# Performance work log

Measured on AMD Instinct MI355X. Metric: run time of the kernel, lower is better.

## Reference

```python
import jax, jax.numpy as jnp
import numpy as np

VOCAB, EMB = 100000, 50
KERNEL_NUM, SIGMA, EXACT_SIGMA = 21, 0.1, 0.001
OUT_LAYERS = [10, 5]


def _kernel_params():
    # Mirrors KNRM._get_kernels_layers
    mus = [1.0]
    bin_size = 2.0 / (KERNEL_NUM - 1)
    mus.append(1 - bin_size / 2)
    for i in range(1, KERNEL_NUM - 1):
        mus.append(mus[i] - bin_size)
    mus = list(reversed(mus))
    sigmas = [SIGMA] * (KERNEL_NUM - 1) + [EXACT_SIGMA]
    return np.array(mus, np.float32), np.array(sigmas, np.float32)

MUS, SIGMAS = _kernel_params()


def setup_inputs() -> dict:
    key = jax.random.key(0)
    ks = jax.random.split(key, 12)
    B, LQ, LD = 2048, 32, 256
    emb = jax.random.normal(ks[0], (VOCAB, EMB), jnp.float32)
    emb = emb.at[0].set(0.0)  # padding_idx=0
    query1 = jax.random.randint(ks[1], (B, LQ), 0, VOCAB)
    doc1 = jax.random.randint(ks[2], (B, LD), 0, VOCAB)
    query2 = jax.random.randint(ks[3], (B, LQ), 0, VOCAB)
    doc2 = jax.random.randint(ks[4], (B, LD), 0, VOCAB)
    def lin(k, fan_in, fan_out):
        bound = 1.0 / np.sqrt(fan_in)
        kw, kb = jax.random.split(k)
        w = jax.random.uniform(kw, (fan_out, fan_in), jnp.float32, -bound, bound)
        b = jax.random.uniform(kb, (fan_out,), jnp.float32, -bound, bound)
        return w, b
    w0, b0 = lin(ks[5], KERNEL_NUM, OUT_LAYERS[0])
    w1, b1 = lin(ks[6], OUT_LAYERS[0], OUT_LAYERS[1])
    w2, b2 = lin(ks[7], OUT_LAYERS[1], 1)
    return dict(emb=emb, w0=w0, b0=b0, w1=w1, b1=b1, w2=w2, b2=b2,
                query1=query1, doc1=doc1, query2=query2, doc2=doc2)


def _matching_matrix(emb, query, doc):
    qe = emb[query]                     # [B, Lq, E]
    de = emb[doc]                       # [B, Ld, E]
    qn = qe / (jnp.linalg.norm(qe, axis=-1, keepdims=True) + 1e-13)
    dn = de / (jnp.linalg.norm(de, axis=-1, keepdims=True) + 1e-13)
    return jnp.einsum('bqe,bde->bqd', qn, dn)  # cosine sim [B, Lq, Ld]


def _apply_kernels(mm):
    # Loop over the fixed 21 kernels (structurally distinct mu/sigma),
    # avoiding a [B,Lq,Ld,21] intermediate, as the original does.
    km = []
    for mu, sg in zip(MUS, SIGMAS):
        k = jnp.exp(-(mm - mu) ** 2 / (2.0 * sg * sg))
        km.append(jnp.log1p(k.sum(axis=-1)).sum(axis=-1))  # [B]
    return jnp.stack(km, axis=1)  # [B, K]


def _mlp(x, w0, b0, w1, b1, w2, b2):
    h = jax.nn.relu(x @ w0.T + b0)
    h = jax.nn.relu(h @ w1.T + b1)
    return h @ w2.T + b2  # [B, 1]


def _predict(emb, w0, b0, w1, b1, w2, b2, query, doc):
    mm = _matching_matrix(emb, query, doc)
    ko = _apply_kernels(mm)
    return _mlp(ko, w0, b0, w1, b1, w2, b2)


def reference(emb, w0, b0, w1, b1, w2, b2, query1, doc1, query2, doc2):
    logits1 = _predict(emb, w0, b0, w1, b1, w2, b2, query1, doc1)
    logits2 = _predict(emb, w0, b0, w1, b1, w2, b2, query2, doc2)
    return jax.nn.sigmoid(logits1 - logits2)  # [B, 1]
```

## Files before the change

kernel.cpp:

```cpp
#include <hip/hip_runtime.h>
#include <hip/hip_fp16.h>

#define EMB_N 50
#define KP 64
#define LQ 32
#define LD 256
#define KN 21
#define MMH 36
#define BATCH 2048

typedef short v8s __attribute__((ext_vector_type(8)));
typedef float v4f __attribute__((ext_vector_type(4)));
typedef float v2f __attribute__((ext_vector_type(2)));

#define PK_ACC(d, b)    asm("v_pk_add_f32 %0, %0, %1" : "+v"(d) : "v"(b))
#define PK_MULA(d, b)   asm("v_pk_mul_f32 %0, %0, %1" : "+v"(d) : "v"(b))

__device__ inline short bf16_rne(float f) {
  unsigned u = __float_as_uint(f);
  unsigned r = u + 0x7fffu + ((u >> 16) & 1u);
  return (short)(r >> 16);
}
__device__ inline float bf16_tof(short h) {
  return __uint_as_float(((unsigned)(unsigned short)h) << 16);
}

__global__ __launch_bounds__(256) void vocab_norm_kernel(
    const float* __restrict__ emb, short* __restrict__ vb,
    short* __restrict__ vlo, int vocab)
{
  int gid = blockIdx.x * 256 + threadIdx.x;
  int r = gid >> 3;
  int c = gid & 7;
  if (r >= vocab) return;
  const float* row = emb + (size_t)r * EMB_N;
  float v[8];
#pragma unroll
  for (int k = 0; k < 8; k++) v[k] = 0.f;
  float ss = 0.f;
  int e0 = c * 8;
  if (c < 6) {
    const float2* p = (const float2*)(row + e0);
#pragma unroll
    for (int k = 0; k < 4; k++) {
      float2 t = p[k];
      v[2*k] = t.x; v[2*k+1] = t.y;
      ss = fmaf(t.x, t.x, ss); ss = fmaf(t.y, t.y, ss);
    }
  } else if (c == 6) {
    float2 t = *(const float2*)(row + 48);
    v[0] = t.x; v[1] = t.y;
    ss = fmaf(t.x, t.x, t.y * t.y);
  }
  ss += __shfl_xor(ss, 1);
  ss += __shfl_xor(ss, 2);
  ss += __shfl_xor(ss, 4);
  float inv = 1.0f / (sqrtf(ss) + 1e-13f);
  short hi[8], lo[8];
#pragma unroll
  for (int k = 0; k < 8; k++) {
    float f = v[k] * inv;
    hi[k] = bf16_rne(f);
    lo[k] = bf16_rne(f - bf16_tof(hi[k]));
  }
  size_t o = (size_t)r * KP + e0;
  *(uint4*)(vb + o)  = *(const uint4*)hi;
  *(uint4*)(vlo + o) = *(const uint4*)lo;
}

__device__ __constant__ const float CJ[KN] = {
  2.5261639e-20f, 2.0469719e-16f, 6.1019363e-13f, 6.6915861e-10f, 2.6995785e-7f,
  4.0065297e-5f,  2.1874911e-3f,  4.3936937e-2f,  0.32465247f,    0.88249690f,
  0.88249690f,    0.32465247f,    4.3936937e-2f,  2.1874911e-3f,  4.0065297e-5f,
  2.6995785e-7f,  6.6915861e-10f, 6.1019363e-13f, 2.0469719e-16f, 2.5261639e-20f,
  1.0f
};

__global__ __launch_bounds__(256, 6) void knrm_main_kernel(
    const short* __restrict__ vb, const short* __restrict__ vlo,
    const int* __restrict__ q1, const int* __restrict__ d1,
    const int* __restrict__ q2, const int* __restrict__ d2,
    const float* __restrict__ w0, const float* __restrict__ b0,
    const float* __restrict__ w1, const float* __restrict__ b1,
    const float* __restrict__ w2, const float* __restrict__ b2,
    float* __restrict__ lgbuf)
{
  __shared__ unsigned short mmh[LD * MMH];
  __shared__ float Sq[LQ][KN + 1];
  __shared__ float ko[KN];
  __shared__ float h0s[10];
  __shared__ float h1s[5];

  const int pair = blockIdx.x >> 11;
  const int b = blockIdx.x & (BATCH - 1);
  const int tid = threadIdx.x;
  const int wave = tid >> 6;
  const int lane = tid & 63;
  const int l15 = lane & 15;
  const int quad = lane >> 4;

  const int* qp = pair ? q2 : q1;
  const int* dp = pair ? d2 : d1;

  if (tid < KN) ko[tid] = 0.f;
  if (tid < LQ) Sq[tid][20] = 0.f;

  int mydtok = dp[b * LD + tid];

  const int mtile = wave & 1;
  const int n0 = (wave >> 1) * 8;

  int qtok = qp[b * LQ + mtile * 16 + l15];
  const short* qh = vb  + (size_t)qtok * KP + quad * 8;
  const short* ql = vlo + (size_t)qtok * KP + quad * 8;
  v8s Ah0 = *(const v8s*)(qh);
  v8s Ah1 = *(const v8s*)(qh + 32);
  v8s Al0 = *(const v8s*)(ql);
  v8s Al1 = *(const v8s*)(ql + 32);

  int dtoks[8];
#pragma unroll
  for (int n = 0; n < 8; n++)
    dtoks[n] = dp[b * LD + (n0 + n) * 16 + l15];

#pragma unroll 2
  for (int n = 0; n < 8; n++) {
    int dtok = dtoks[n];
    const short* dh = vb + (size_t)dtok * KP + quad * 8;
    v8s B0 = *(const v8s*)(dh);
    v8s B1 = *(const v8s*)(dh + 32);
    v4f C = {0.f, 0.f, 0.f, 0.f};
    C = __builtin_amdgcn_mfma_f32_16x16x32_bf16(Ah0, B0, C, 0, 0, 0);
    C = __builtin_amdgcn_mfma_f32_16x16x32_bf16(Ah1, B1, C, 0, 0, 0);
    C = __builtin_amdgcn_mfma_f32_16x16x32_bf16(Al0, B0, C, 0, 0, 0);
    C = __builtin_amdgcn_mfma_f32_16x16x32_bf16(Al1, B1, C, 0, 0, 0);
    int col = (n0 + n) * 16 + l15;
    int row0 = mtile * 16 + quad * 4;
    __half2 h01 = __floats2half2_rn(C[0], C[1]);
    __half2 h23 = __floats2half2_rn(C[2], C[3]);
    uint2 wpk;
    wpk.x = *reinterpret_cast<unsigned*>(&h01);
    wpk.y = *reinterpret_cast<unsigned*>(&h23);
    *(uint2*)&mmh[col * MMH + row0] = wpk;
  }
  __syncthreads();

#pragma unroll
  for (int qq = 0; qq < LQ; qq++) {
    int qt = qp[b * LQ + qq];
    unsigned long long m = __ballot(mydtok == qt && qt != 0);
    if (lane == 0 && m)
      atomicAdd(&Sq[qq][20], (float)__popcll(m));
  }

  const int q  = tid >> 3;
  const int db = tid & 7;
  v2f U2[10];
#pragma unroll
  for (int i = 0; i < 10; i++) U2[i] = (v2f){0.f, 0.f};

#pragma unroll 4
  for (int i = 0; i < LD / 8; i++) {
    float x = __half2float(*reinterpret_cast<const __half*>(
                  &mmh[(db + 8 * i) * MMH + q]));
    float gc = __builtin_amdgcn_exp2f(x * fmaf(-72.1347520f, x, 7.2134752f));
    float ex = 14.4269504f * x;
    float r  = __builtin_amdgcn_exp2f(ex);
    float ri = __builtin_amdgcn_exp2f(-ex);
    v2f p  = {gc, gc * ri};
    v2f rr = {r, ri};
#pragma unroll
    for (int k2 = 0; k2 < 10; k2++) {
      PK_ACC(U2[k2], p);
      PK_MULA(p, rr);
    }
  }

#pragma unroll
  for (int j = 0; j < 20; j++) {
    float v = (j < 10) ? U2[9 - j].y : U2[j - 10].x;
    v += __shfl_xor(v, 1);
    v += __shfl_xor(v, 2);
    v += __shfl_xor(v, 4);
    if (db == 0) Sq[q][j] = v;
  }
  __syncthreads();

  {
    int qq = tid & 31;
    int jb = tid >> 5;
#pragma unroll
    for (int k = 0; k < 3; k++) {
      int j = jb + 8 * k;
      if (j < KN) {
        float y = fmaf(CJ[j], Sq[qq][j], 1.0f);
        float l = 0.69314718f * __builtin_amdgcn_logf(y);
        atomicAdd(&ko[j], l);
      }
    }
  }
  __syncthreads();

  if (tid < 10) {
    float h = b0[tid];
#pragma unroll
    for (int k = 0; k < KN; k++) h = fmaf(w0[tid * KN + k], ko[k], h);
    h0s[tid] = fmaxf(h, 0.f);
  }
  __syncthreads();
  if (tid < 5) {
    float h = b1[tid];
#pragma unroll
    for (int k = 0; k < 10; k++) h = fmaf(w1[tid * 10 + k], h0s[k], h);
    h1s[tid] = fmaxf(h, 0.f);
  }
  __syncthreads();
  if (tid == 0) {
    float h = b2[0];
#pragma unroll
    for (int k = 0; k < 5; k++) h = fmaf(w2[k], h1s[k], h);
    lgbuf[pair * BATCH + b] = h;
  }
}

__global__ __launch_bounds__(256) void knrm_combine_kernel(
    const float* __restrict__ lgbuf, float* __restrict__ out)
{
  int i = blockIdx.x * 256 + threadIdx.x;
  if (i < BATCH) {
    float z = lgbuf[i] - lgbuf[BATCH + i];
    out[i] = 1.0f / (1.0f + expf(-z));
  }
}

extern "C" void kernel_launch(void* const* d_in, const int* in_sizes, int n_in,
                              void* d_out, int out_size, void* d_ws, size_t ws_size,
                              hipStream_t stream)
{
  const float* emb = (const float*)d_in[0];
  const float* w0  = (const float*)d_in[1];
  const float* b0  = (const float*)d_in[2];
  const float* w1  = (const float*)d_in[3];
  const float* b1  = (const float*)d_in[4];
  const float* w2  = (const float*)d_in[5];
  const float* b2  = (const float*)d_in[6];
  const int* q1 = (const int*)d_in[7];
  const int* dd1 = (const int*)d_in[8];
  const int* q2 = (const int*)d_in[9];
  const int* dd2 = (const int*)d_in[10];
  float* out = (float*)d_out;

  int vocab = in_sizes[0] / EMB_N;
  int B = in_sizes[7] / LQ;

  float* lgbuf = (float*)d_ws;
  short* vb  = (short*)(lgbuf + 2 * BATCH);
  short* vlo = vb + (size_t)vocab * KP;

  vocab_norm_kernel<<<(vocab * 8 + 255) / 256, 256, 0, stream>>>(emb, vb, vlo, vocab);
  knrm_main_kernel<<<2 * B, 256, 0, stream>>>(vb, vlo, q1, dd1, q2, dd2,
                                              w0, b0, w1, b1, w2, b2, lgbuf);
  knrm_combine_kernel<<<(B + 255) / 256, 256, 0, stream>>>(lgbuf, out);
}
```

Measured before the change: 157.7 us.

## Fuse kernel-pooling into MFMA loop, drop shared similarity matrix

The kernel no longer stores the fp16 cosine-similarity matrix in shared memory and re-reads it. Each wave now applies the Gaussian kernel accumulation directly to its MFMA output registers. Operand roles are swapped so doc tokens are the A operand, and the next doc embedding is prefetched while the current one is processed. Partial sums are reduced with cross-lane shuffles into a small shared array, and the log-sum into ko uses shuffle reductions instead of shared atomics. The occupancy hint drops from 6 to 5 because register pressure rises, and every element now goes through the exp work in fp32 rather than via a half-precision round trip.

```diff
diff --git a/kernel.cpp b/kernel.cpp
--- a/kernel.cpp
+++ b/kernel.cpp
@@ -1,12 +1,10 @@
 #include <hip/hip_runtime.h>
-#include <hip/hip_fp16.h>
 
 #define EMB_N 50
 #define KP 64
 #define LQ 32
 #define LD 256
 #define KN 21
-#define MMH 36
 #define BATCH 2048
 
 typedef short v8s __attribute__((ext_vector_type(8)));
@@ -76,7 +74,7 @@
   1.0f
 };
 
-__global__ __launch_bounds__(256, 6) void knrm_main_kernel(
+__global__ __launch_bounds__(256, 5) void knrm_main_kernel(
     const short* __restrict__ vb, const short* __restrict__ vlo,
     const int* __restrict__ q1, const int* __restrict__ d1,
     const int* __restrict__ q2, const int* __restrict__ d2,
@@ -85,8 +83,8 @@
     const float* __restrict__ w2, const float* __restrict__ b2,
     float* __restrict__ lgbuf)
 {
-  __shared__ unsigned short mmh[LD * MMH];
-  __shared__ float Sq[LQ][KN + 1];
+  __shared__ float part[4][16][KN];
+  __shared__ float Sqex[LQ];
   __shared__ float ko[KN];
   __shared__ float h0s[10];
   __shared__ float h1s[5];
@@ -98,51 +96,28 @@
   const int lane = tid & 63;
   const int l15 = lane & 15;
   const int quad = lane >> 4;
+  const int qtile = wave >> 1;
+  const int thalf = wave & 1;
 
   const int* qp = pair ? q2 : q1;
   const int* dp = pair ? d2 : d1;
 
-  if (tid < KN) ko[tid] = 0.f;
-  if (tid < LQ) Sq[tid][20] = 0.f;
-
-  int mydtok = dp[b * LD + tid];
-
-  const int mtile = wave & 1;
-  const int n0 = (wave >> 1) * 8;
-
-  int qtok = qp[b * LQ + mtile * 16 + l15];
+  if (tid < LQ) Sqex[tid] = 0.f;
+
+  int qtok = qp[b * LQ + qtile * 16 + l15];
   const short* qh = vb  + (size_t)qtok * KP + quad * 8;
   const short* ql = vlo + (size_t)qtok * KP + quad * 8;
-  v8s Ah0 = *(const v8s*)(qh);
-  v8s Ah1 = *(const v8s*)(qh + 32);
-  v8s Al0 = *(const v8s*)(ql);
-  v8s Al1 = *(const v8s*)(ql + 32);
-
+  v8s Bh0 = *(const v8s*)(qh);
+  v8s Bh1 = *(const v8s*)(qh + 32);
+  v8s Bl0 = *(const v8s*)(ql);
+  v8s Bl1 = *(const v8s*)(ql + 32);
+
+  int mydtok = dp[b * LD + tid];
   int dtoks[8];
 #pragma unroll
-  for (int n = 0; n < 8; n++)
-    dtoks[n] = dp[b * LD + (n0 + n) * 16 + l15];
-
-#pragma unroll 2
-  for (int n = 0; n < 8; n++) {
-    int dtok = dtoks[n];
-    const short* dh = vb + (size_t)dtok * KP + quad * 8;
-    v8s B0 = *(const v8s*)(dh);
-    v8s B1 = *(const v8s*)(dh + 32);
-    v4f C = {0.f, 0.f, 0.f, 0.f};
-    C = __builtin_amdgcn_mfma_f32_16x16x32_bf16(Ah0, B0, C, 0, 0, 0);
-    C = __builtin_amdgcn_mfma_f32_16x16x32_bf16(Ah1, B1, C, 0, 0, 0);
-    C = __builtin_amdgcn_mfma_f32_16x16x32_bf16(Al0, B0, C, 0, 0, 0);
-    C = __builtin_amdgcn_mfma_f32_16x16x32_bf16(Al1, B1, C, 0, 0, 0);
-    int col = (n0 + n) * 16 + l15;
-    int row0 = mtile * 16 + quad * 4;
-    __half2 h01 = __floats2half2_rn(C[0], C[1]);
-    __half2 h23 = __floats2half2_rn(C[2], C[3]);
-    uint2 wpk;
-    wpk.x = *reinterpret_cast<unsigned*>(&h01);
-    wpk.y = *reinterpret_cast<unsigned*>(&h23);
-    *(uint2*)&mmh[col * MMH + row0] = wpk;
-  }
+  for (int t = 0; t < 8; t++)
+    dtoks[t] = dp[b * LD + (thalf * 8 + t) * 16 + l15];
+
   __syncthreads();
 
 #pragma unroll
@@ -150,53 +125,78 @@
     int qt = qp[b * LQ + qq];
     unsigned long long m = __ballot(mydtok == qt && qt != 0);
     if (lane == 0 && m)
-      atomicAdd(&Sq[qq][20], (float)__popcll(m));
-  }
-
-  const int q  = tid >> 3;
-  const int db = tid & 7;
+      atomicAdd(&Sqex[qq], (float)__popcll(m));
+  }
+
   v2f U2[10];
 #pragma unroll
   for (int i = 0; i < 10; i++) U2[i] = (v2f){0.f, 0.f};
 
-#pragma unroll 4
-  for (int i = 0; i < LD / 8; i++) {
-    float x = __half2float(*reinterpret_cast<const __half*>(
-                  &mmh[(db + 8 * i) * MMH + q]));
-    float gc = __builtin_amdgcn_exp2f(x * fmaf(-72.1347520f, x, 7.2134752f));
-    float ex = 14.4269504f * x;
-    float r  = __builtin_amdgcn_exp2f(ex);
-    float ri = __builtin_amdgcn_exp2f(-ex);
-    v2f p  = {gc, gc * ri};
-    v2f rr = {r, ri};
-#pragma unroll
-    for (int k2 = 0; k2 < 10; k2++) {
-      PK_ACC(U2[k2], p);
-      PK_MULA(p, rr);
-    }
-  }
-
-#pragma unroll
-  for (int j = 0; j < 20; j++) {
-    float v = (j < 10) ? U2[9 - j].y : U2[j - 10].x;
-    v += __shfl_xor(v, 1);
-    v += __shfl_xor(v, 2);
-    v += __shfl_xor(v, 4);
-    if (db == 0) Sq[q][j] = v;
+  const short* dptr0 = vb + (size_t)dtoks[0] * KP + quad * 8;
+  v8s A0 = *(const v8s*)(dptr0);
+  v8s A1 = *(const v8s*)(dptr0 + 32);
+
+#pragma unroll 2
+  for (int t = 0; t < 8; t++) {
+    v8s N0, N1;
+    if (t < 7) {
+      const short* dptr = vb + (size_t)dtoks[t + 1] * KP + quad * 8;
+      N0 = *(const v8s*)(dptr);
+      N1 = *(const v8s*)(dptr + 32);
+    }
+    v4f C = {0.f, 0.f, 0.f, 0.f};
+    C = __builtin_amdgcn_mfma_f32_16x16x32_bf16(A0, Bh0, C, 0, 0, 0);
+    C = __builtin_amdgcn_mfma_f32_16x16x32_bf16(A1, Bh1, C, 0, 0, 0);
+    C = __builtin_amdgcn_mfma_f32_16x16x32_bf16(A0, Bl0, C, 0, 0, 0);
+    C = __builtin_amdgcn_mfma_f32_16x16x32_bf16(A1, Bl1, C, 0, 0, 0);
+#pragma unroll
+    for (int r = 0; r < 4; r++) {
+      float x = C[r];
+      float gc = __builtin_amdgcn_exp2f(x * fmaf(-72.1347520f, x, 7.2134752f));
+      float ex = 14.4269504f * x;
+      float rr1 = __builtin_amdgcn_exp2f(ex);
+      float ri  = __builtin_amdgcn_exp2f(-ex);
+      v2f p  = {gc, gc * ri};
+      v2f rr = {rr1, ri};
+#pragma unroll
+      for (int k2 = 0; k2 < 10; k2++) {
+        PK_ACC(U2[k2], p);
+        PK_MULA(p, rr);
+      }
+    }
+    if (t < 7) { A0 = N0; A1 = N1; }
+  }
+
+#pragma unroll
+  for (int i = 0; i < 10; i++) {
+    float ux = U2[i].x, uy = U2[i].y;
+    ux += __shfl_xor(ux, 16);  uy += __shfl_xor(uy, 16);
+    ux += __shfl_xor(ux, 32);  uy += __shfl_xor(uy, 32);
+    if (quad == 0) {
+      part[wave][l15][10 + i] = ux;
+      part[wave][l15][9 - i]  = uy;
+    }
   }
   __syncthreads();
 
   {
     int qq = tid & 31;
+    int qi = qq & 15, qt2 = qq >> 4;
     int jb = tid >> 5;
 #pragma unroll
     for (int k = 0; k < 3; k++) {
       int j = jb + 8 * k;
+      float l = 0.f;
       if (j < KN) {
-        float y = fmaf(CJ[j], Sq[qq][j], 1.0f);
-        float l = 0.69314718f * __builtin_amdgcn_logf(y);
-        atomicAdd(&ko[j], l);
+        float s = (j < 20) ? part[qt2 * 2][qi][j] + part[qt2 * 2 + 1][qi][j]
+                           : Sqex[qq];
+        float y = fmaf(CJ[j], s, 1.0f);
+        l = 0.69314718f * __builtin_amdgcn_logf(y);
       }
+      l += __shfl_xor(l, 1);  l += __shfl_xor(l, 2);
+      l += __shfl_xor(l, 4);  l += __shfl_xor(l, 8);
+      l += __shfl_xor(l, 16);
+      if (qq == 0 && j < KN) ko[j] = l;
     }
   }
   __syncthreads();
```

New measurement: 141.5 us. -10.2%, faster.
